# Kernel tuning notes

Measured on AMD Instinct MI355X. Metric: run time of the kernel, lower is better.

Reference implementation:

```python
import jax, jax.numpy as jnp
import numpy as np

N_NODES = 50000
N_EDGES = 800000
FEAT_DIM = 16
HIDDEN = 128
N_LAYERS = 4
OUT_DIM = 12
N_GRAPHS = 1024

def setup_inputs() -> dict:
    key = jax.random.key(0)
    ks = jax.random.split(key, 8)
    return {
        "x": jax.random.normal(ks[0], (N_NODES, FEAT_DIM), jnp.float32),
        "edge_index": jax.random.randint(ks[1], (2, N_EDGES), 0, N_NODES, dtype=jnp.int32),
        "edge_attr": jnp.zeros((N_EDGES, 4), jnp.float32),
        "batch_idx": jnp.sort(jax.random.randint(ks[2], (N_NODES,), 0, N_GRAPHS, dtype=jnp.int32)),
        # node-embed MLP: Linear(16,128) -> relu -> Linear(128,128)
        "W_e1": jax.random.normal(ks[3], (FEAT_DIM, HIDDEN), jnp.float32) * 0.1,
        "b_e1": jnp.zeros((HIDDEN,), jnp.float32),
        "W_e2": jax.random.normal(ks[4], (HIDDEN, HIDDEN), jnp.float32) * 0.05,
        "b_e2": jnp.zeros((HIDDEN,), jnp.float32),
        # stacked GCNConv weights/biases for 4 layers
        "W_g": jax.random.normal(ks[5], (N_LAYERS, HIDDEN, HIDDEN), jnp.float32) * 0.05,
        "b_g": jnp.zeros((N_LAYERS, HIDDEN), jnp.float32),
        # output Linear(128,12)
        "W_o": jax.random.normal(ks[6], (HIDDEN, OUT_DIM), jnp.float32) * 0.05,
        "b_o": jnp.zeros((OUT_DIM,), jnp.float32),
    }

def _gcn_layer(h_in, src, dst, W, b):
    # PyG GCNConv with add_self_loops=True, symmetric normalization:
    # out_i = sum_{j in N(i) u {i}} (d_i d_j)^{-1/2} (x_j W) + b
    h = h_in @ W                                   # [N, H]
    deg = jnp.zeros((N_NODES,), h.dtype).at[dst].add(1.0) + 1.0  # +1 self-loop
    dinv = jax.lax.rsqrt(deg)                      # [N]
    norm = dinv[src] * dinv[dst]                   # [E]
    msg = h[src] * norm[:, None]                   # gather + scale  [E, H]
    agg = jnp.zeros_like(h).at[dst].add(msg)       # scatter-add to targets
    agg = agg + h * (dinv * dinv)[:, None]         # self-loop term
    return agg + b

def reference(x, edge_index, edge_attr, batch_idx, W_e1, b_e1, W_e2, b_e2, W_g, b_g, W_o, b_o):
    del edge_attr  # use_edge_attribution=False; GCNConv ignores edge features
    src, dst = edge_index[0], edge_index[1]
    # node embedding MLP
    h = jax.nn.relu(x @ W_e1 + b_e1) @ W_e2 + b_e2
    for i in range(N_LAYERS):
        h = jax.nn.relu(_gcn_layer(h, src, dst, W_g[i], b_g[i]))
        # dropout is identity in eval mode
    # scatter-mean pooling over graphs
    sums = jax.ops.segment_sum(h, batch_idx, num_segments=N_GRAPHS)
    cnts = jax.ops.segment_sum(jnp.ones((N_NODES,), h.dtype), batch_idx, num_segments=N_GRAPHS)
    pooled = sums / jnp.maximum(cnts, 1.0)[:, None]
    return pooled @ W_o + b_o
```

## Files before the change

### kernel.cpp

```cpp
#include <hip/hip_runtime.h>

#define N_NODES 50000
#define N_EDGES 800000
#define FEAT    16
#define HID     128
#define NLAYERS 4
#define OUTD    12
#define NGRAPH  1024
#define SCAN_NB 196

__device__ inline float4 f4zero() { return make_float4(0.f, 0.f, 0.f, 0.f); }
__device__ inline float4 f4fma(float a, float4 w, float4 acc) {
    acc.x = fmaf(a, w.x, acc.x);
    acc.y = fmaf(a, w.y, acc.y);
    acc.z = fmaf(a, w.z, acc.z);
    acc.w = fmaf(a, w.w, acc.w);
    return acc;
}
__device__ inline float4 f4add(float4 a, float4 b) {
    return make_float4(a.x + b.x, a.y + b.y, a.z + b.z, a.w + b.w);
}
__device__ inline float4 f4relu(float4 a) {
    return make_float4(fmaxf(a.x, 0.f), fmaxf(a.y, 0.f), fmaxf(a.z, 0.f), fmaxf(a.w, 0.f));
}

__global__ void k_deg(const int* __restrict__ ei, int* __restrict__ degi) {
    int e = blockIdx.x * 256 + threadIdx.x;
    if (e < N_EDGES) atomicAdd(&degi[ei[N_EDGES + e]], 1);
}

__global__ void k_dinv(const int* __restrict__ degi, float* __restrict__ dinv) {
    int i = blockIdx.x * 256 + threadIdx.x;
    if (i < N_NODES) dinv[i] = rsqrtf((float)degi[i] + 1.0f);
}

__global__ void k_scan_part(const int* __restrict__ degi, int* __restrict__ part) {
    __shared__ int s[256];
    int t = threadIdx.x;
    int i = blockIdx.x * 256 + t;
    int v = (i < N_NODES) ? degi[i] : 0;
    s[t] = v;
    __syncthreads();
    for (int st = 128; st > 0; st >>= 1) {
        if (t < st) s[t] += s[t + st];
        __syncthreads();
    }
    if (t == 0) part[blockIdx.x] = s[0];
}

__global__ void k_scan_mid(int* __restrict__ part) {
    __shared__ int s[256];
    int t = threadIdx.x;
    int v = (t < SCAN_NB) ? part[t] : 0;
    s[t] = v;
    __syncthreads();
    for (int st = 1; st < 256; st <<= 1) {
        int u = (t >= st) ? s[t - st] : 0;
        __syncthreads();
        s[t] += u;
        __syncthreads();
    }
    if (t < SCAN_NB) part[t] = s[t] - v;
}

__global__ void k_scan_final(const int* __restrict__ degi, const int* __restrict__ part,
                             int* __restrict__ offs) {
    __shared__ int s[256];
    int t = threadIdx.x;
    int i = blockIdx.x * 256 + t;
    int v = (i < N_NODES) ? degi[i] : 0;
    s[t] = v;
    __syncthreads();
    for (int st = 1; st < 256; st <<= 1) {
        int u = (t >= st) ? s[t - st] : 0;
        __syncthreads();
        s[t] += u;
        __syncthreads();
    }
    if (i <= N_NODES) offs[i] = s[t] - v + part[blockIdx.x];
}

__global__ void k_fill(const int* __restrict__ ei, const int* __restrict__ offs,
                       const float* __restrict__ dinv,
                       int* __restrict__ cursor, int2* __restrict__ erec) {
    int e = blockIdx.x * 256 + threadIdx.x;
    if (e < N_EDGES) {
        int srcv = ei[e];
        int dstv = ei[N_EDGES + e];
        int p = atomicAdd(&cursor[dstv], 1);
        erec[offs[dstv] + p] = make_int2(srcv, __float_as_int(dinv[srcv]));
    }
}

#define GM 64
__global__ void __launch_bounds__(256) k_embed_fused(
        const float* __restrict__ x,
        const float* __restrict__ W1, const float* __restrict__ b1,
        const float* __restrict__ W2, const float* __restrict__ b2,
        float* __restrict__ outp) {
    __shared__ float x_l[GM][FEAT];
    __shared__ float a_l[GM][HID];
    int t = threadIdx.x;
    long n0 = (long)blockIdx.x * GM;
    {
        int r  = t >> 2;
        int c4 = (t & 3) << 2;
        long n = n0 + r;
        float4 v = (n < N_NODES) ? *(const float4*)&x[n * FEAT + c4] : f4zero();
        *(float4*)&x_l[r][c4] = v;
    }
    __syncthreads();
    int fgrp = t & 31, ngrp = t >> 5;
    int f4 = fgrp << 2;
    {
        float4 acc[8];
#pragma unroll
        for (int r = 0; r < 8; ++r) acc[r] = f4zero();
#pragma unroll
        for (int k4 = 0; k4 < 4; ++k4) {
            float4 wv[4];
#pragma unroll
            for (int kk = 0; kk < 4; ++kk)
                wv[kk] = *(const float4*)&W1[(k4 * 4 + kk) * HID + f4];
            float4 xv[8];
#pragma unroll
            for (int r = 0; r < 8; ++r)
                xv[r] = *(const float4*)&x_l[ngrp * 8 + r][k4 << 2];
#pragma unroll
            for (int r = 0; r < 8; ++r) {
                acc[r] = f4fma(xv[r].x, wv[0], acc[r]);
                acc[r] = f4fma(xv[r].y, wv[1], acc[r]);
                acc[r] = f4fma(xv[r].z, wv[2], acc[r]);
                acc[r] = f4fma(xv[r].w, wv[3], acc[r]);
            }
        }
        float4 bv = *(const float4*)&b1[f4];
#pragma unroll
        for (int r = 0; r < 8; ++r)
            *(float4*)&a_l[ngrp * 8 + r][f4] = f4relu(f4add(acc[r], bv));
    }
    __syncthreads();
    float4 acc[8];
#pragma unroll
    for (int r = 0; r < 8; ++r) acc[r] = f4zero();
#pragma unroll 4
    for (int k4 = 0; k4 < 32; ++k4) {
        float4 wv[4];
#pragma unroll
        for (int kk = 0; kk < 4; ++kk)
            wv[kk] = *(const float4*)&W2[(k4 * 4 + kk) * HID + f4];
        float4 av[8];
#pragma unroll
        for (int r = 0; r < 8; ++r)
            av[r] = *(const float4*)&a_l[ngrp * 8 + r][k4 << 2];
#pragma unroll
        for (int r = 0; r < 8; ++r) {
            acc[r] = f4fma(av[r].x, wv[0], acc[r]);
            acc[r] = f4fma(av[r].y, wv[1], acc[r]);
            acc[r] = f4fma(av[r].z, wv[2], acc[r]);
            acc[r] = f4fma(av[r].w, wv[3], acc[r]);
        }
    }
    float4 bv = *(const float4*)&b2[f4];
#pragma unroll
    for (int r = 0; r < 8; ++r) {
        long n = n0 + ngrp * 8 + r;
        if (n < N_NODES) *(float4*)&outp[n * HID + f4] = f4add(acc[r], bv);
    }
}

__global__ void __launch_bounds__(256) k_gemm(
        const float* __restrict__ A, const float* __restrict__ W,
        float* __restrict__ B) {
    __shared__ float a_l[GM][HID];
    int t = threadIdx.x;
    long n0 = (long)blockIdx.x * GM;
#pragma unroll
    for (int i = 0; i < 8; ++i) {
        int p  = t + 256 * i;
        int r  = p >> 5;
        int c4 = (p & 31) << 2;
        long n = n0 + r;
        float4 v = (n < N_NODES) ? *(const float4*)&A[n * HID + c4] : f4zero();
        *(float4*)&a_l[r][c4] = v;
    }
    __syncthreads();
    int fgrp = t & 31, ngrp = t >> 5;
    int f4 = fgrp << 2;
    float4 acc[8];
#pragma unroll
    for (int r = 0; r < 8; ++r) acc[r] = f4zero();
#pragma unroll 4
    for (int k4 = 0; k4 < 32; ++k4) {
        float4 wv[4];
#pragma unroll
        for (int kk = 0; kk < 4; ++kk)
            wv[kk] = *(const float4*)&W[(k4 * 4 + kk) * HID + f4];
        float4 av[8];
#pragma unroll
        for (int r = 0; r < 8; ++r)
            av[r] = *(const float4*)&a_l[ngrp * 8 + r][k4 << 2];
#pragma unroll
        for (int r = 0; r < 8; ++r) {
            acc[r] = f4fma(av[r].x, wv[0], acc[r]);
            acc[r] = f4fma(av[r].y, wv[1], acc[r]);
            acc[r] = f4fma(av[r].z, wv[2], acc[r]);
            acc[r] = f4fma(av[r].w, wv[3], acc[r]);
        }
    }
#pragma unroll
    for (int r = 0; r < 8; ++r) {
        long n = n0 + ngrp * 8 + r;
        if (n < N_NODES) *(float4*)&B[n * HID + f4] = acc[r];
    }
}

__global__ void __launch_bounds__(256) k_agg(
        const float* __restrict__ hp,
        const int2* __restrict__ erec, const int* __restrict__ offs,
        const float* __restrict__ dinv, const float* __restrict__ bias,
        float* __restrict__ hout) {
    int t = threadIdx.x;
    int lane = t & 63;
    int w = t >> 6;
    int i = blockIdx.x * 4 + w;
    if (i >= N_NODES) return;
    float di = dinv[i];
    int s0 = offs[i], s1 = offs[i + 1];
    const float2* hp2 = (const float2*)hp;
    float2 self = hp2[(long)i * 64 + lane];
    float2 bv = ((const float2*)bias)[lane];
    float ax = fmaf(di * di, self.x, bv.x);
    float ay = fmaf(di * di, self.y, bv.y);
    for (int base = s0; base < s1; base += 64) {
        int n = s1 - base; if (n > 64) n = 64;
        int last = n - 1;
        int2 e = (lane < n) ? erec[base + lane] : make_int2(0, 0);
        int   sv_l = e.x;
        float nm_l = __int_as_float(e.y);
        for (int k = 0; k < n; k += 16) {
            int a[16]; float m[16];
#pragma unroll
            for (int u = 0; u < 16; ++u) {
                int kk = k + u;
                int ks = kk < last ? kk : last;
                a[u] = __shfl(sv_l, ks);
                float mu = __shfl(nm_l, ks);
                m[u] = (kk < n) ? mu * di : 0.f;
            }
            float2 v[16];
#pragma unroll
            for (int u = 0; u < 16; ++u) v[u] = hp2[(long)a[u] * 64 + lane];
#pragma unroll
            for (int u = 0; u < 16; ++u) {
                ax = fmaf(m[u], v[u].x, ax);
                ay = fmaf(m[u], v[u].y, ay);
            }
        }
    }
    float2 r;
    r.x = fmaxf(ax, 0.f);
    r.y = fmaxf(ay, 0.f);
    ((float2*)hout)[(long)i * 64 + lane] = r;
}

#define PN 16
__global__ void __launch_bounds__(256) k_pool(
        const float* __restrict__ h, const int* __restrict__ batch,
        float* __restrict__ pooled, float* __restrict__ cnt) {
    int t = threadIdx.x;
    int lane = t & 31, grp = t >> 5;
    long n0 = ((long)blockIdx.x * 8 + grp) * PN;
    if (n0 >= N_NODES) return;
    long n1 = n0 + PN; if (n1 > N_NODES) n1 = N_NODES;
    const float4* h4 = (const float4*)h;
    float4 run = f4zero();
    int curg = batch[n0];
    int c = 0;
    for (long n = n0; n < n1; ++n) {
        int g = batch[n];
        if (g != curg) {
            float* pb = &pooled[(long)curg * HID + (lane << 2)];
            atomicAdd(pb + 0, run.x); atomicAdd(pb + 1, run.y);
            atomicAdd(pb + 2, run.z); atomicAdd(pb + 3, run.w);
            if (lane == 0) atomicAdd(&cnt[curg], (float)c);
            run = f4zero(); c = 0; curg = g;
        }
        run = f4add(run, h4[n * 32 + lane]);
        ++c;
    }
    float* pb = &pooled[(long)curg * HID + (lane << 2)];
    atomicAdd(pb + 0, run.x); atomicAdd(pb + 1, run.y);
    atomicAdd(pb + 2, run.z); atomicAdd(pb + 3, run.w);
    if (lane == 0) atomicAdd(&cnt[curg], (float)c);
}

__global__ void __launch_bounds__(HID) k_out(
        const float* __restrict__ pooled, const float* __restrict__ cnt,
        const float* __restrict__ Wo, const float* __restrict__ bo,
        float* __restrict__ out) {
    __shared__ float p[HID];
    int g = blockIdx.x;
    int f = threadIdx.x;
    float inv = 1.0f / fmaxf(cnt[g], 1.0f);
    p[f] = pooled[g * HID + f] * inv;
    __syncthreads();
    if (f < OUTD) {
        float acc = bo[f];
#pragma unroll 8
        for (int k = 0; k < HID; ++k) acc += p[k] * Wo[k * OUTD + f];
        out[g * OUTD + f] = acc;
    }
}

extern "C" void kernel_launch(void* const* d_in, const int* in_sizes, int n_in,
                              void* d_out, int out_size, void* d_ws, size_t ws_size,
                              hipStream_t stream) {
    const float* x    = (const float*)d_in[0];
    const int*   ei   = (const int*)d_in[1];
    const int*   bidx = (const int*)d_in[3];
    const float* We1  = (const float*)d_in[4];
    const float* be1  = (const float*)d_in[5];
    const float* We2  = (const float*)d_in[6];
    const float* be2  = (const float*)d_in[7];
    const float* Wg   = (const float*)d_in[8];
    const float* bg   = (const float*)d_in[9];
    const float* Wo   = (const float*)d_in[10];
    const float* bo   = (const float*)d_in[11];
    float* out = (float*)d_out;

    char* ws = (char*)d_ws;
    size_t o = 0;
    auto take = [&](size_t bytes) { size_t r = o; o += (bytes + 255) & ~(size_t)255; return r; };
    size_t off_degi   = take((size_t)N_NODES * 4);
    size_t off_cursor = take((size_t)N_NODES * 4);
    size_t off_pooled = take((size_t)NGRAPH * HID * 4);
    size_t off_cnt    = take((size_t)NGRAPH * 4);
    size_t zero_bytes = o;
    size_t off_dinv   = take((size_t)N_NODES * 4);
    size_t off_offs   = take((size_t)(N_NODES + 1) * 4);
    size_t off_part   = take((size_t)256 * 4);
    size_t off_erec   = take((size_t)N_EDGES * 8);
    size_t off_hA     = take((size_t)N_NODES * HID * 4);
    size_t off_hB     = take((size_t)N_NODES * HID * 4);

    int*   degi   = (int*)(ws + off_degi);
    int*   cursor = (int*)(ws + off_cursor);
    float* pooled = (float*)(ws + off_pooled);
    float* cnt    = (float*)(ws + off_cnt);
    float* dinv   = (float*)(ws + off_dinv);
    int*   offs   = (int*)(ws + off_offs);
    int*   part   = (int*)(ws + off_part);
    int2*  erec   = (int2*)(ws + off_erec);
    float* hA     = (float*)(ws + off_hA);
    float* hB     = (float*)(ws + off_hB);

    hipMemsetAsync(d_ws, 0, zero_bytes, stream);

    k_deg<<<(N_EDGES + 255) / 256, 256, 0, stream>>>(ei, degi);
    k_dinv<<<(N_NODES + 255) / 256, 256, 0, stream>>>(degi, dinv);
    k_scan_part<<<SCAN_NB, 256, 0, stream>>>(degi, part);
    k_scan_mid<<<1, 256, 0, stream>>>(part);
    k_scan_final<<<SCAN_NB, 256, 0, stream>>>(degi, part, offs);
    k_fill<<<(N_EDGES + 255) / 256, 256, 0, stream>>>(ei, offs, dinv, cursor, erec);

    int gemm_grid = (N_NODES + GM - 1) / GM;
    k_embed_fused<<<gemm_grid, 256, 0, stream>>>(x, We1, be1, We2, be2, hA);

    for (int l = 0; l < NLAYERS; ++l) {
        k_gemm<<<gemm_grid, 256, 0, stream>>>(hA, Wg + (size_t)l * HID * HID, hB);
        k_agg<<<(N_NODES + 3) / 4, 256, 0, stream>>>(hB, erec, offs, dinv,
                                                     bg + (size_t)l * HID, hA);
    }

    k_pool<<<(N_NODES + 8 * PN - 1) / (8 * PN), 256, 0, stream>>>(hA, bidx, pooled, cnt);
    k_out<<<NGRAPH, HID, 0, stream>>>(pooled, cnt, Wo, bo, out);
}
```

Measured before the change: 601.9 us.

## Fuse dinv into scan, shrink agg unroll, merge pooling with output via binary search

Computes dinv inside the scan partial kernel, removing one launch. Halves the gather unroll in the aggregation kernel from 16 to 8, which lowers register pressure but means fewer loads in flight per wave. Replaces the atomic pooling kernel and the output kernel with one kernel per graph that binary-searches the sorted batch index for its node range and sums rows directly. This drops the pooled/cnt buffers and their atomics at the cost of serial per-graph row loops.

```diff
diff --git a/kernel.cpp b/kernel.cpp
--- a/kernel.cpp
+++ b/kernel.cpp
@@ -29,16 +29,13 @@
     if (e < N_EDGES) atomicAdd(&degi[ei[N_EDGES + e]], 1);
 }
 
-__global__ void k_dinv(const int* __restrict__ degi, float* __restrict__ dinv) {
-    int i = blockIdx.x * 256 + threadIdx.x;
-    if (i < N_NODES) dinv[i] = rsqrtf((float)degi[i] + 1.0f);
-}
-
-__global__ void k_scan_part(const int* __restrict__ degi, int* __restrict__ part) {
+__global__ void k_scan_part(const int* __restrict__ degi, int* __restrict__ part,
+                            float* __restrict__ dinv) {
     __shared__ int s[256];
     int t = threadIdx.x;
     int i = blockIdx.x * 256 + t;
     int v = (i < N_NODES) ? degi[i] : 0;
+    if (i < N_NODES) dinv[i] = rsqrtf((float)v + 1.0f);
     s[t] = v;
     __syncthreads();
     for (int st = 128; st > 0; st >>= 1) {
@@ -238,21 +235,21 @@
         int2 e = (lane < n) ? erec[base + lane] : make_int2(0, 0);
         int   sv_l = e.x;
         float nm_l = __int_as_float(e.y);
-        for (int k = 0; k < n; k += 16) {
-            int a[16]; float m[16];
-#pragma unroll
-            for (int u = 0; u < 16; ++u) {
+        for (int k = 0; k < n; k += 8) {
+            int a[8]; float m[8];
+#pragma unroll
+            for (int u = 0; u < 8; ++u) {
                 int kk = k + u;
                 int ks = kk < last ? kk : last;
                 a[u] = __shfl(sv_l, ks);
                 float mu = __shfl(nm_l, ks);
                 m[u] = (kk < n) ? mu * di : 0.f;
             }
-            float2 v[16];
-#pragma unroll
-            for (int u = 0; u < 16; ++u) v[u] = hp2[(long)a[u] * 64 + lane];
-#pragma unroll
-            for (int u = 0; u < 16; ++u) {
+            float2 v[8];
+#pragma unroll
+            for (int u = 0; u < 8; ++u) v[u] = hp2[(long)a[u] * 64 + lane];
+#pragma unroll
+            for (int u = 0; u < 8; ++u) {
                 ax = fmaf(m[u], v[u].x, ax);
                 ay = fmaf(m[u], v[u].y, ay);
             }
@@ -264,52 +261,35 @@
     ((float2*)hout)[(long)i * 64 + lane] = r;
 }
 
-#define PN 16
-__global__ void __launch_bounds__(256) k_pool(
+__global__ void __launch_bounds__(HID) k_poolout(
         const float* __restrict__ h, const int* __restrict__ batch,
-        float* __restrict__ pooled, float* __restrict__ cnt) {
-    int t = threadIdx.x;
-    int lane = t & 31, grp = t >> 5;
-    long n0 = ((long)blockIdx.x * 8 + grp) * PN;
-    if (n0 >= N_NODES) return;
-    long n1 = n0 + PN; if (n1 > N_NODES) n1 = N_NODES;
-    const float4* h4 = (const float4*)h;
-    float4 run = f4zero();
-    int curg = batch[n0];
-    int c = 0;
-    for (long n = n0; n < n1; ++n) {
-        int g = batch[n];
-        if (g != curg) {
-            float* pb = &pooled[(long)curg * HID + (lane << 2)];
-            atomicAdd(pb + 0, run.x); atomicAdd(pb + 1, run.y);
-            atomicAdd(pb + 2, run.z); atomicAdd(pb + 3, run.w);
-            if (lane == 0) atomicAdd(&cnt[curg], (float)c);
-            run = f4zero(); c = 0; curg = g;
-        }
-        run = f4add(run, h4[n * 32 + lane]);
-        ++c;
-    }
-    float* pb = &pooled[(long)curg * HID + (lane << 2)];
-    atomicAdd(pb + 0, run.x); atomicAdd(pb + 1, run.y);
-    atomicAdd(pb + 2, run.z); atomicAdd(pb + 3, run.w);
-    if (lane == 0) atomicAdd(&cnt[curg], (float)c);
-}
-
-__global__ void __launch_bounds__(HID) k_out(
-        const float* __restrict__ pooled, const float* __restrict__ cnt,
         const float* __restrict__ Wo, const float* __restrict__ bo,
         float* __restrict__ out) {
     __shared__ float p[HID];
+    __shared__ int range[2];
     int g = blockIdx.x;
     int f = threadIdx.x;
-    float inv = 1.0f / fmaxf(cnt[g], 1.0f);
-    p[f] = pooled[g * HID + f] * inv;
+    if (f < 2) {
+        int key = g + f;
+        int lo = 0, hi = N_NODES;
+        while (lo < hi) {
+            int mid = (lo + hi) >> 1;
+            if (batch[mid] < key) lo = mid + 1; else hi = mid;
+        }
+        range[f] = lo;
+    }
+    __syncthreads();
+    int n0 = range[0], n1 = range[1];
+    float acc = 0.f;
+    for (int n = n0; n < n1; ++n) acc += h[(long)n * HID + f];
+    float inv = 1.0f / fmaxf((float)(n1 - n0), 1.0f);
+    p[f] = acc * inv;
     __syncthreads();
     if (f < OUTD) {
-        float acc = bo[f];
+        float o = bo[f];
 #pragma unroll 8
-        for (int k = 0; k < HID; ++k) acc += p[k] * Wo[k * OUTD + f];
-        out[g * OUTD + f] = acc;
+        for (int k = 0; k < HID; ++k) o = fmaf(p[k], Wo[k * OUTD + f], o);
+        out[g * OUTD + f] = o;
     }
 }
 
@@ -334,8 +314,6 @@
     auto take = [&](size_t bytes) { size_t r = o; o += (bytes + 255) & ~(size_t)255; return r; };
     size_t off_degi   = take((size_t)N_NODES * 4);
     size_t off_cursor = take((size_t)N_NODES * 4);
-    size_t off_pooled = take((size_t)NGRAPH * HID * 4);
-    size_t off_cnt    = take((size_t)NGRAPH * 4);
     size_t zero_bytes = o;
     size_t off_dinv   = take((size_t)N_NODES * 4);
     size_t off_offs   = take((size_t)(N_NODES + 1) * 4);
@@ -346,8 +324,6 @@
 
     int*   degi   = (int*)(ws + off_degi);
     int*   cursor = (int*)(ws + off_cursor);
-    float* pooled = (float*)(ws + off_pooled);
-    float* cnt    = (float*)(ws + off_cnt);
     float* dinv   = (float*)(ws + off_dinv);
     int*   offs   = (int*)(ws + off_offs);
     int*   part   = (int*)(ws + off_part);
@@ -358,21 +334,19 @@
     hipMemsetAsync(d_ws, 0, zero_bytes, stream);
 
     k_deg<<<(N_EDGES + 255) / 256, 256, 0, stream>>>(ei, degi);
-    k_dinv<<<(N_NODES + 255) / 256, 256, 0, stream>>>(degi, dinv);
-    k_scan_part<<<SCAN_NB, 256, 0, stream>>>(degi, part);
+    k_scan_part<<<SCAN_NB, 256, 0, stream>>>(degi, part, dinv);
     k_scan_mid<<<1, 256, 0, stream>>>(part);
     k_scan_final<<<SCAN_NB, 256, 0, stream>>>(degi, part, offs);
     k_fill<<<(N_EDGES + 255) / 256, 256, 0, stream>>>(ei, offs, dinv, cursor, erec);
 
-    int gemm_grid = (N_NODES + GM - 1) / GM;
-    k_embed_fused<<<gemm_grid, 256, 0, stream>>>(x, We1, be1, We2, be2, hA);
+    int tile_grid = (N_NODES + GM - 1) / GM;
+    k_embed_fused<<<tile_grid, 256, 0, stream>>>(x, We1, be1, We2, be2, hA);
 
     for (int l = 0; l < NLAYERS; ++l) {
-        k_gemm<<<gemm_grid, 256, 0, stream>>>(hA, Wg + (size_t)l * HID * HID, hB);
+        k_gemm<<<tile_grid, 256, 0, stream>>>(hA, Wg + (size_t)l * HID * HID, hB);
         k_agg<<<(N_NODES + 3) / 4, 256, 0, stream>>>(hB, erec, offs, dinv,
                                                      bg + (size_t)l * HID, hA);
     }
 
-    k_pool<<<(N_NODES + 8 * PN - 1) / (8 * PN), 256, 0, stream>>>(hA, bidx, pooled, cnt);
-    k_out<<<NGRAPH, HID, 0, stream>>>(pooled, cnt, Wo, bo, out);
-}
+    k_poolout<<<NGRAPH, HID, 0, stream>>>(hA, bidx, Wo, bo, out);
+}
```

Result: no change. 598.1 us (-0.6%).
